# Kernel tuning notes

Hardware: AMD Instinct MI355X
Metric: run time of the kernel (lower is better)

Reference implementation:

```python
import jax, jax.numpy as jnp
import numpy as np

ASSIGN_RATIO = 0.1  # hard-coded inside coarsen_graph in the original
EPS_CUT = 1e-7
EPS_NORM = 1e-12  # torch F.normalize eps


def _normalize_batch_adj(adj):
    # adj: [B, N, N]
    n = adj.shape[1]
    A = adj + jnp.eye(n, dtype=adj.dtype)
    deg_inv_sqrt = jnp.clip(A.sum(-1), 1.0, None) ** -0.5  # [B, N]
    newA = deg_inv_sqrt[..., :, None] * A * deg_inv_sqrt[..., None, :]
    row_mask = (adj.sum(-1) > 0).astype(adj.dtype)  # [B, N]
    return row_mask[..., :, None] * newA


def setup_inputs():
    key = jax.random.key(0)
    k0, k1, k2, k3, k4 = jax.random.split(key, 5)
    B, N, D, T = 512, 128, 256, 512
    concept_hidden = jax.random.normal(k0, (B, N, D), jnp.float32)
    adj = jax.random.uniform(k1, (B, N, N), jnp.float32)
    head = jax.random.randint(k2, (B, T), 0, N)
    lin_w = jax.random.normal(k3, (1, D), jnp.float32) / np.sqrt(D).astype(np.float32)
    bias = jax.random.normal(k4, (1,), jnp.float32)
    return {"concept_hidden": concept_hidden, "adj": adj, "head": head,
            "lin_w": lin_w, "bias": bias}


def reference(concept_hidden, adj, head, lin_w, bias):
    # concept_hidden: [B, N, D], adj: [B, N, N], head: [B, T] node indices
    x = concept_hidden
    B, N, D = x.shape

    out = x @ lin_w.T                      # [B, N, 1]  self.lin(x)
    norm_adj = _normalize_batch_adj(adj)   # [B, N, N]
    out = norm_adj @ out + bias            # [B, N, 1]
    alpha = jax.nn.sigmoid(out ** 2)[..., 0]  # [B, N]

    # batch_num_nodes[i] = len(set(head[i]))  -> count unique via sort
    hs = jnp.sort(head, axis=-1)
    n_uniq = 1 + (hs[:, 1:] != hs[:, :-1]).sum(-1)  # [B]

    # per-sample k = ceil(n * 0.1) + 1 (only when n > 1); cut = k-th largest alpha
    k = jnp.ceil(n_uniq.astype(jnp.float32) * ASSIGN_RATIO).astype(jnp.int32) + 1
    a_desc = jnp.sort(alpha, axis=-1)[:, ::-1]       # descending
    idx = jnp.clip(k - 1, 0, N - 1)
    cut = jnp.take_along_axis(a_desc, idx[:, None], axis=-1)[:, 0]
    cut = jnp.where(n_uniq > 1, cut, jnp.zeros_like(cut))  # [B]

    cut_alpha = jax.nn.relu(alpha + EPS_CUT - cut[:, None])  # [B, N]

    # S = norm_adj * cut_alpha broadcast over rows, then L1-normalize rows
    S = norm_adj * cut_alpha[:, None, :]
    S = S / jnp.clip(jnp.abs(S).sum(-1, keepdims=True), EPS_NORM, None)

    St = jnp.swapaxes(S, 1, 2)             # [B, N, N]
    embedding_tensor = St @ x              # S^T x   [B, N, D]
    new_adj = (St @ adj) @ S               # S^T A S [B, N, N]
    return embedding_tensor, new_adj
```

## Files before the change

### kernel.cpp

```cpp
#include <hip/hip_runtime.h>

#define Bsz 512
#define Nn  128
#define Dd  256
#define Tt  512

typedef __attribute__((ext_vector_type(8))) short short8;
typedef __attribute__((ext_vector_type(4))) float f32x4;

__device__ __forceinline__ ushort f2bf(float f) {
    union { float f; unsigned u; } v; v.f = f;
    unsigned r = v.u + 0x7fffu + ((v.u >> 16) & 1u);
    return (ushort)(r >> 16);
}
__device__ __forceinline__ unsigned pk2(float a, float b) {
    return (unsigned)f2bf(a) | ((unsigned)f2bf(b) << 16);
}

__global__ __launch_bounds__(256) void xprep(
    const float* __restrict__ x, const float* __restrict__ lin_w,
    float* __restrict__ dotv2, ushort* __restrict__ xT)
{
    const int h = blockIdx.x, b = blockIdx.y;
    __shared__ float xbufT[32][130];
    __shared__ float pdot[128][8];
    __shared__ float wS[128];
    const int t = threadIdx.x;
    if (t < 128) wS[t] = lin_w[h * 128 + t];
    const int c4 = t & 7;
    const int kb = t >> 3;
    const int kc = t & 15, dsub = t >> 4;
    float p[4] = {0.f, 0.f, 0.f, 0.f};
    __syncthreads();

    for (int c = 0; c < 4; ++c) {
        const int dl = 4 * c4;
        float4 v[4];
#pragma unroll
        for (int i = 0; i < 4; ++i)
            v[i] = *(const float4*)&x[((size_t)b * Nn + (kb + 32 * i)) * Dd
                                      + h * 128 + c * 32 + dl];
        const float w0 = wS[c*32+dl],   w1 = wS[c*32+dl+1];
        const float w2 = wS[c*32+dl+2], w3 = wS[c*32+dl+3];
#pragma unroll
        for (int i = 0; i < 4; ++i) {
            p[i] += v[i].x*w0 + v[i].y*w1 + v[i].z*w2 + v[i].w*w3;
            xbufT[dl    ][kb + 32*i] = v[i].x;
            xbufT[dl + 1][kb + 32*i] = v[i].y;
            xbufT[dl + 2][kb + 32*i] = v[i].z;
            xbufT[dl + 3][kb + 32*i] = v[i].w;
        }
        __syncthreads();
#pragma unroll
        for (int pp = 0; pp < 2; ++pp) {
            int d = dsub + 16 * pp;
            float2 q0 = *(float2*)&xbufT[d][kc*8 + 0];
            float2 q1 = *(float2*)&xbufT[d][kc*8 + 2];
            float2 q2 = *(float2*)&xbufT[d][kc*8 + 4];
            float2 q3 = *(float2*)&xbufT[d][kc*8 + 6];
            uint4 pkv;
            pkv.x = pk2(q0.x, q0.y);
            pkv.y = pk2(q1.x, q1.y);
            pkv.z = pk2(q2.x, q2.y);
            pkv.w = pk2(q3.x, q3.y);
            *(uint4*)&xT[((size_t)b * Dd + h * 128 + c * 32 + d) * Nn + kc * 8] = pkv;
        }
        __syncthreads();
    }
#pragma unroll
    for (int i = 0; i < 4; ++i) pdot[kb + 32*i][c4] = p[i];
    __syncthreads();
    if (t < 128) {
        float s = 0.f;
#pragma unroll
        for (int j = 0; j < 8; ++j) s += pdot[t][j];
        dotv2[((size_t)b * Nn + t) * 2 + h] = s;
    }
}

__global__ __launch_bounds__(256) void sprep(
    const float* __restrict__ adj, const int* __restrict__ head,
    const float* __restrict__ dotv2, const float* __restrict__ bias,
    ushort* __restrict__ STbf)
{
    const int b = blockIdx.x;
    __shared__ __align__(16) float adjS[Nn][132];
    __shared__ __align__(16) float ttS[Nn], disS[Nn], maskS[Nn],
                                   alphaS[Nn], uS[Nn], rowcS[Nn];
    __shared__ float partS[Nn][2];
    __shared__ int   flags[Nn];
    __shared__ int   nuniq_s;
    __shared__ float cut_s;

    const int t = threadIdx.x;
    const float bias0 = bias[0];
    if (t < Nn) flags[t] = 0;
    if (t == 0) { nuniq_s = 0; cut_s = 0.f; }

    const float* adjb = adj + (size_t)b * (Nn * Nn);
#pragma unroll
    for (int i = 0; i < 16; ++i) {
        int f = t + 256 * i;
        int rr = f >> 5, c = (f & 31) * 4;
        *(float4*)&adjS[rr][c] = *(const float4*)&adjb[rr * Nn + c];
    }
    __syncthreads();

    {
        int h0 = head[(size_t)b * Tt + t];
        int h1 = head[(size_t)b * Tt + 256 + t];
        flags[h0] = 1; flags[h1] = 1;
    }

    const int r = t >> 1, hh = t & 1, base = hh * 64;
    {
        float4 s4 = {0.f, 0.f, 0.f, 0.f};
#pragma unroll
        for (int j = 0; j < 16; ++j) {
            float4 v = *(float4*)&adjS[r][base + 4*j];
            s4.x += v.x; s4.y += v.y; s4.z += v.z; s4.w += v.w;
        }
        partS[r][hh] = (s4.x + s4.y) + (s4.z + s4.w);
    }
    __syncthreads();
    if (t < Nn) {
        float rs  = partS[t][0] + partS[t][1];
        float m   = (rs > 0.f) ? 1.f : 0.f;
        float dis = 1.f / sqrtf(fmaxf(rs + 1.f, 1.f));
        maskS[t] = m; disS[t] = dis;
        float lin = dotv2[((size_t)b * Nn + t) * 2]
                  + dotv2[((size_t)b * Nn + t) * 2 + 1];
        ttS[t] = dis * lin;
        atomicAdd(&nuniq_s, flags[t]);
    }
    __syncthreads();
    {
        float4 a = {0.f, 0.f, 0.f, 0.f};
#pragma unroll
        for (int j = 0; j < 16; ++j) {
            float4 v = *(float4*)&adjS[r][base + 4*j];
            float4 w = *(float4*)&ttS[base + 4*j];
            a.x += v.x*w.x; a.y += v.y*w.y; a.z += v.z*w.z; a.w += v.w*w.w;
        }
        partS[r][hh] = (a.x + a.y) + (a.z + a.w);
    }
    __syncthreads();
    if (t < Nn) {
        float mv = partS[t][0] + partS[t][1];
        float o  = maskS[t] * disS[t] * (mv + ttS[t]) + bias0;
        alphaS[t] = 1.f / (1.f + expf(-o * o));
    }
    __syncthreads();
    if (t < Nn) {
        int nu = nuniq_s;
        if (nu > 1) {
            int idx = (int)ceilf((float)nu * 0.1f);
            if (idx > Nn - 1) idx = Nn - 1;
            float an = alphaS[t];
            int cg = 0, ce = 0;
            for (int j = 0; j < Nn; ++j) {
                float aj = alphaS[j];
                cg += (aj > an); ce += (aj == an);
            }
            if (cg <= idx && idx < cg + ce) cut_s = an;
        }
    }
    __syncthreads();
    if (t < Nn) uS[t] = fmaxf(alphaS[t] + 1e-7f - cut_s, 0.f) * disS[t];
    __syncthreads();
    {
        float4 a = {0.f, 0.f, 0.f, 0.f};
#pragma unroll
        for (int j = 0; j < 16; ++j) {
            float4 v = *(float4*)&adjS[r][base + 4*j];
            float4 w = *(float4*)&uS[base + 4*j];
            a.x += v.x*w.x; a.y += v.y*w.y; a.z += v.z*w.z; a.w += v.w*w.w;
        }
        partS[r][hh] = (a.x + a.y) + (a.z + a.w);
    }
    __syncthreads();
    if (t < Nn) {
        float tot  = partS[t][0] + partS[t][1] + uS[t];
        float rsum = maskS[t] * disS[t] * tot;
        rowcS[t] = maskS[t] * disS[t] / fmaxf(rsum, 1e-12f);
    }
    __syncthreads();
    {
        const float um = uS[r];
        ushort* outp = STbf + ((size_t)b * Nn + r) * Nn + base;
#pragma unroll
        for (int kcc = 0; kcc < 8; ++kcc) {
            int k0 = base + kcc * 8;
            float vv[8];
#pragma unroll
            for (int j = 0; j < 8; ++j) {
                int k = k0 + j;
                vv[j] = rowcS[k] * (adjS[k][r] + ((k == r) ? 1.f : 0.f)) * um;
            }
            uint4 pkv;
            pkv.x = pk2(vv[0], vv[1]); pkv.y = pk2(vv[2], vv[3]);
            pkv.z = pk2(vv[4], vv[5]); pkv.w = pk2(vv[6], vv[7]);
            *(uint4*)(outp + kcc * 8) = pkv;
        }
    }
}

__global__ __launch_bounds__(256, 2) void emb_gemm(
    const ushort* __restrict__ STbf, const ushort* __restrict__ xT,
    float* __restrict__ emb)
{
    const int d0 = blockIdx.x * 128;
    const int b  = blockIdx.y;
    __shared__ ushort STl[128][136];
    __shared__ ushort xTl[128][136];
    const int t = threadIdx.x;
    const uint4* sg = (const uint4*)(STbf + (size_t)b * Nn * Nn);
    const uint4* xg = (const uint4*)(xT + ((size_t)b * Dd + d0) * Nn);
#pragma unroll
    for (int i = 0; i < 8; ++i) {
        int f = t + 256 * i;
        int row = f >> 4, c8 = f & 15;
        *(uint4*)&STl[row][c8 * 8] = sg[f];
        *(uint4*)&xTl[row][c8 * 8] = xg[f];
    }
    __syncthreads();

    const int lane = t & 63, wv = t >> 6;
    const int l15 = lane & 15, quad = lane >> 4;
    const int m0 = wv * 32;
    f32x4 acc[2][8];
#pragma unroll
    for (int mt = 0; mt < 2; ++mt)
#pragma unroll
        for (int nt = 0; nt < 8; ++nt) acc[mt][nt] = (f32x4){0.f, 0.f, 0.f, 0.f};

#pragma unroll
    for (int k0 = 0; k0 < 128; k0 += 32) {
        short8 a0 = *(const short8*)&STl[m0 + l15][k0 + quad * 8];
        short8 a1 = *(const short8*)&STl[m0 + 16 + l15][k0 + quad * 8];
        short8 bf[8];
#pragma unroll
        for (int nt = 0; nt < 8; ++nt)
            bf[nt] = *(const short8*)&xTl[nt * 16 + l15][k0 + quad * 8];
#pragma unroll
        for (int nt = 0; nt < 8; ++nt) {
            acc[0][nt] = __builtin_amdgcn_mfma_f32_16x16x32_bf16(a0, bf[nt], acc[0][nt], 0, 0, 0);
            acc[1][nt] = __builtin_amdgcn_mfma_f32_16x16x32_bf16(a1, bf[nt], acc[1][nt], 0, 0, 0);
        }
    }
#pragma unroll
    for (int mt = 0; mt < 2; ++mt)
#pragma unroll
        for (int nt = 0; nt < 8; ++nt)
#pragma unroll
            for (int rr = 0; rr < 4; ++rr) {
                int row = m0 + mt * 16 + quad * 4 + rr;
                int col = d0 + nt * 16 + l15;
                emb[((size_t)b * Nn + row) * Dd + col] = acc[mt][nt][rr];
            }
}

__global__ __launch_bounds__(256, 2) void padj_gemm(
    const float* __restrict__ adj, const ushort* __restrict__ STbf,
    float* __restrict__ nadj)
{
    const int b = blockIdx.x;
    __shared__ ushort bufA[128][136];
    __shared__ ushort STl[128][136];
    const int t = threadIdx.x;

    const float* adjb = adj + (size_t)b * Nn * Nn;
#pragma unroll
    for (int i = 0; i < 16; ++i) {
        int f = t + 256 * i;
        int rr = f >> 5, c4 = f & 31;
        float4 v = *(const float4*)&adjb[rr * Nn + c4 * 4];
        uint2 w; w.x = pk2(v.x, v.y); w.y = pk2(v.z, v.w);
        *(uint2*)&bufA[rr][c4 * 4] = w;
    }
    const uint4* sg = (const uint4*)(STbf + (size_t)b * Nn * Nn);
#pragma unroll
    for (int i = 0; i < 8; ++i) {
        int f = t + 256 * i;
        *(uint4*)&STl[f >> 4][(f & 15) * 8] = sg[f];
    }
    __syncthreads();

    const int lane = t & 63, wv = t >> 6;
    const int l15 = lane & 15, quad = lane >> 4;
    const int m0 = wv * 32;
    f32x4 acc[2][8];
#pragma unroll
    for (int mt = 0; mt < 2; ++mt)
#pragma unroll
        for (int nt = 0; nt < 8; ++nt) acc[mt][nt] = (f32x4){0.f, 0.f, 0.f, 0.f};

#pragma unroll
    for (int k0 = 0; k0 < 128; k0 += 32) {
        short8 a0 = *(const short8*)&bufA[m0 + l15][k0 + quad * 8];
        short8 a1 = *(const short8*)&bufA[m0 + 16 + l15][k0 + quad * 8];
        short8 bf[8];
#pragma unroll
        for (int nt = 0; nt < 8; ++nt)
            bf[nt] = *(const short8*)&STl[nt * 16 + l15][k0 + quad * 8];
#pragma unroll
        for (int nt = 0; nt < 8; ++nt) {
            acc[0][nt] = __builtin_amdgcn_mfma_f32_16x16x32_bf16(a0, bf[nt], acc[0][nt], 0, 0, 0);
            acc[1][nt] = __builtin_amdgcn_mfma_f32_16x16x32_bf16(a1, bf[nt], acc[1][nt], 0, 0, 0);
        }
    }
    __syncthreads();
#pragma unroll
    for (int mt = 0; mt < 2; ++mt)
#pragma unroll
        for (int nt = 0; nt < 8; ++nt) {
            int j    = nt * 16 + l15;
            int mcol = m0 + mt * 16 + quad * 4;
            uint2 w;
            w.x = pk2(acc[mt][nt][0], acc[mt][nt][1]);
            w.y = pk2(acc[mt][nt][2], acc[mt][nt][3]);
            *(uint2*)&bufA[j][mcol] = w;
        }
    __syncthreads();

#pragma unroll
    for (int mt = 0; mt < 2; ++mt)
#pragma unroll
        for (int nt = 0; nt < 8; ++nt) acc[mt][nt] = (f32x4){0.f, 0.f, 0.f, 0.f};

#pragma unroll
    for (int k0 = 0; k0 < 128; k0 += 32) {
        short8 a0 = *(const short8*)&STl[m0 + l15][k0 + quad * 8];
        short8 a1 = *(const short8*)&STl[m0 + 16 + l15][k0 + quad * 8];
        short8 bf[8];
#pragma unroll
        for (int nt = 0; nt < 8; ++nt)
            bf[nt] = *(const short8*)&bufA[nt * 16 + l15][k0 + quad * 8];
#pragma unroll
        for (int nt = 0; nt < 8; ++nt) {
            acc[0][nt] = __builtin_amdgcn_mfma_f32_16x16x32_bf16(a0, bf[nt], acc[0][nt], 0, 0, 0);
            acc[1][nt] = __builtin_amdgcn_mfma_f32_16x16x32_bf16(a1, bf[nt], acc[1][nt], 0, 0, 0);
        }
    }
#pragma unroll
    for (int mt = 0; mt < 2; ++mt)
#pragma unroll
        for (int nt = 0; nt < 8; ++nt)
#pragma unroll
            for (int rr = 0; rr < 4; ++rr) {
                int row = m0 + mt * 16 + quad * 4 + rr;
                int col = nt * 16 + l15;
                nadj[((size_t)b * Nn + row) * Nn + col] = acc[mt][nt][rr];
            }
}

extern "C" void kernel_launch(void* const* d_in, const int* in_sizes, int n_in,
                              void* d_out, int out_size, void* d_ws, size_t ws_size,
                              hipStream_t stream)
{
    const float* x     = (const float*)d_in[0];
    const float* adj   = (const float*)d_in[1];
    const int*   head  = (const int*)d_in[2];
    const float* lin_w = (const float*)d_in[3];
    const float* bias  = (const float*)d_in[4];

    float* emb  = (float*)d_out;
    float* nadj = emb + (size_t)Bsz * Nn * Dd;

    ushort* STbf = (ushort*)d_ws;
    ushort* xT   = STbf + (size_t)Bsz * Nn * Nn;
    float*  dotv2 = (float*)(xT + (size_t)Bsz * Dd * Nn);

    xprep<<<dim3(2, Bsz), 256, 0, stream>>>(x, lin_w, dotv2, xT);
    sprep<<<Bsz, 256, 0, stream>>>(adj, head, dotv2, bias, STbf);
    emb_gemm<<<dim3(2, Bsz), 256, 0, stream>>>(STbf, xT, emb);
    padj_gemm<<<Bsz, 256, 0, stream>>>(adj, STbf, nadj);
}
```

Baseline: 230.6 us.

## Fuse four per-batch kernels into one mega kernel keeping S and adj in LDS

Merges xprep, sprep, emb_gemm and padj_gemm into a single kernel with one block per batch. The fp32 adjacency stays in shared memory and S^T goes straight to LDS as bf16, so the global workspace round-trips for STbf, xT and dotv2 and three extra launches disappear. x is read twice (once for the lin dot, once transposed through LDS for the embedding GEMM). This brings less parallelism (512 blocks instead of 1024 for the emb GEMM), larger LDS use per block and a longer serial chain of stages inside each block.

```diff
diff --git a/kernel.cpp b/kernel.cpp
--- a/kernel.cpp
+++ b/kernel.cpp
@@ -16,131 +16,90 @@
 __device__ __forceinline__ unsigned pk2(float a, float b) {
     return (unsigned)f2bf(a) | ((unsigned)f2bf(b) << 16);
 }
-
-__global__ __launch_bounds__(256) void xprep(
-    const float* __restrict__ x, const float* __restrict__ lin_w,
-    float* __restrict__ dotv2, ushort* __restrict__ xT)
+__device__ __forceinline__ short8 pk8(const float* v) {
+    union { uint4 u; short8 s; } c;
+    c.u.x = pk2(v[0], v[1]); c.u.y = pk2(v[2], v[3]);
+    c.u.z = pk2(v[4], v[5]); c.u.w = pk2(v[6], v[7]);
+    return c.s;
+}
+
+__global__ __launch_bounds__(256) void mega(
+    const float* __restrict__ x, const float* __restrict__ adj,
+    const int* __restrict__ head, const float* __restrict__ lin_w,
+    const float* __restrict__ bias,
+    float* __restrict__ emb, float* __restrict__ nadj)
 {
-    const int h = blockIdx.x, b = blockIdx.y;
-    __shared__ float xbufT[32][130];
-    __shared__ float pdot[128][8];
-    __shared__ float wS[128];
-    const int t = threadIdx.x;
-    if (t < 128) wS[t] = lin_w[h * 128 + t];
-    const int c4 = t & 7;
-    const int kb = t >> 3;
-    const int kc = t & 15, dsub = t >> 4;
-    float p[4] = {0.f, 0.f, 0.f, 0.f};
-    __syncthreads();
-
-    for (int c = 0; c < 4; ++c) {
-        const int dl = 4 * c4;
-        float4 v[4];
-#pragma unroll
-        for (int i = 0; i < 4; ++i)
-            v[i] = *(const float4*)&x[((size_t)b * Nn + (kb + 32 * i)) * Dd
-                                      + h * 128 + c * 32 + dl];
-        const float w0 = wS[c*32+dl],   w1 = wS[c*32+dl+1];
-        const float w2 = wS[c*32+dl+2], w3 = wS[c*32+dl+3];
-#pragma unroll
-        for (int i = 0; i < 4; ++i) {
-            p[i] += v[i].x*w0 + v[i].y*w1 + v[i].z*w2 + v[i].w*w3;
-            xbufT[dl    ][kb + 32*i] = v[i].x;
-            xbufT[dl + 1][kb + 32*i] = v[i].y;
-            xbufT[dl + 2][kb + 32*i] = v[i].z;
-            xbufT[dl + 3][kb + 32*i] = v[i].w;
-        }
-        __syncthreads();
-#pragma unroll
-        for (int pp = 0; pp < 2; ++pp) {
-            int d = dsub + 16 * pp;
-            float2 q0 = *(float2*)&xbufT[d][kc*8 + 0];
-            float2 q1 = *(float2*)&xbufT[d][kc*8 + 2];
-            float2 q2 = *(float2*)&xbufT[d][kc*8 + 4];
-            float2 q3 = *(float2*)&xbufT[d][kc*8 + 6];
-            uint4 pkv;
-            pkv.x = pk2(q0.x, q0.y);
-            pkv.y = pk2(q1.x, q1.y);
-            pkv.z = pk2(q2.x, q2.y);
-            pkv.w = pk2(q3.x, q3.y);
-            *(uint4*)&xT[((size_t)b * Dd + h * 128 + c * 32 + d) * Nn + kc * 8] = pkv;
-        }
-        __syncthreads();
-    }
-#pragma unroll
-    for (int i = 0; i < 4; ++i) pdot[kb + 32*i][c4] = p[i];
-    __syncthreads();
-    if (t < 128) {
-        float s = 0.f;
-#pragma unroll
-        for (int j = 0; j < 8; ++j) s += pdot[t][j];
-        dotv2[((size_t)b * Nn + t) * 2 + h] = s;
-    }
-}
-
-__global__ __launch_bounds__(256) void sprep(
-    const float* __restrict__ adj, const int* __restrict__ head,
-    const float* __restrict__ dotv2, const float* __restrict__ bias,
-    ushort* __restrict__ STbf)
-{
-    const int b = blockIdx.x;
-    __shared__ __align__(16) float adjS[Nn][132];
-    __shared__ __align__(16) float ttS[Nn], disS[Nn], maskS[Nn],
-                                   alphaS[Nn], uS[Nn], rowcS[Nn];
+    const int b = blockIdx.x, t = threadIdx.x;
+    __shared__ __align__(16) float bufA[Nn][132];
+    __shared__ __align__(16) ushort STl[Nn][136];
+    __shared__ float wS[Dd];
+    __shared__ float ttS[Nn], disS[Nn], maskS[Nn], alphaS[Nn], uS[Nn], rowcS[Nn];
     __shared__ float partS[Nn][2];
+    __shared__ float dotP[Nn][2];
     __shared__ int   flags[Nn];
-    __shared__ int   nuniq_s;
-    __shared__ float cut_s;
-
-    const int t = threadIdx.x;
+    __shared__ int   nuniq;
+    __shared__ float cutS;
+
     const float bias0 = bias[0];
+    wS[t] = lin_w[t];
     if (t < Nn) flags[t] = 0;
-    if (t == 0) { nuniq_s = 0; cut_s = 0.f; }
-
-    const float* adjb = adj + (size_t)b * (Nn * Nn);
+    if (t == 0) { nuniq = 0; cutS = 0.f; }
+
+    const float* adjb = adj + (size_t)b * Nn * Nn;
 #pragma unroll
     for (int i = 0; i < 16; ++i) {
         int f = t + 256 * i;
         int rr = f >> 5, c = (f & 31) * 4;
-        *(float4*)&adjS[rr][c] = *(const float4*)&adjb[rr * Nn + c];
-    }
-    __syncthreads();
-
-    {
-        int h0 = head[(size_t)b * Tt + t];
-        int h1 = head[(size_t)b * Tt + 256 + t];
-        flags[h0] = 1; flags[h1] = 1;
-    }
-
-    const int r = t >> 1, hh = t & 1, base = hh * 64;
+        *(float4*)&bufA[rr][c] = *(const float4*)&adjb[(size_t)rr * Nn + c];
+    }
+    __syncthreads();
+
+    { int h0 = head[(size_t)b * Tt + t];
+      int h1 = head[(size_t)b * Tt + 256 + t];
+      flags[h0] = 1; flags[h1] = 1; }
+
+    {
+        const int dr = t >> 1, dh = t & 1;
+        const float4* xr = (const float4*)(x + ((size_t)b * Nn + dr) * Dd + dh * 128);
+        float p = 0.f;
+#pragma unroll 8
+        for (int i = 0; i < 32; ++i) {
+            float4 v = xr[i];
+            const float* w = &wS[dh * 128 + 4 * i];
+            p += v.x * w[0] + v.y * w[1] + v.z * w[2] + v.w * w[3];
+        }
+        dotP[dr][dh] = p;
+    }
+
+    const int r = t >> 1, hh = t & 1, cb = hh * 64;
     {
         float4 s4 = {0.f, 0.f, 0.f, 0.f};
 #pragma unroll
         for (int j = 0; j < 16; ++j) {
-            float4 v = *(float4*)&adjS[r][base + 4*j];
+            float4 v = *(float4*)&bufA[r][cb + 4 * j];
             s4.x += v.x; s4.y += v.y; s4.z += v.z; s4.w += v.w;
         }
         partS[r][hh] = (s4.x + s4.y) + (s4.z + s4.w);
     }
     __syncthreads();
+
     if (t < Nn) {
         float rs  = partS[t][0] + partS[t][1];
-        float m   = (rs > 0.f) ? 1.f : 0.f;
+        maskS[t]  = (rs > 0.f) ? 1.f : 0.f;
         float dis = 1.f / sqrtf(fmaxf(rs + 1.f, 1.f));
-        maskS[t] = m; disS[t] = dis;
-        float lin = dotv2[((size_t)b * Nn + t) * 2]
-                  + dotv2[((size_t)b * Nn + t) * 2 + 1];
-        ttS[t] = dis * lin;
-        atomicAdd(&nuniq_s, flags[t]);
-    }
-    __syncthreads();
+        disS[t]   = dis;
+        ttS[t]    = dis * (dotP[t][0] + dotP[t][1]);
+        atomicAdd(&nuniq, flags[t]);
+    }
+    __syncthreads();
+
     {
         float4 a = {0.f, 0.f, 0.f, 0.f};
 #pragma unroll
         for (int j = 0; j < 16; ++j) {
-            float4 v = *(float4*)&adjS[r][base + 4*j];
-            float4 w = *(float4*)&ttS[base + 4*j];
-            a.x += v.x*w.x; a.y += v.y*w.y; a.z += v.z*w.z; a.w += v.w*w.w;
+            float4 v = *(float4*)&bufA[r][cb + 4 * j];
+            float4 w = *(float4*)&ttS[cb + 4 * j];
+            a.x += v.x * w.x; a.y += v.y * w.y; a.z += v.z * w.z; a.w += v.w * w.w;
         }
         partS[r][hh] = (a.x + a.y) + (a.z + a.w);
     }
@@ -152,7 +111,7 @@
     }
     __syncthreads();
     if (t < Nn) {
-        int nu = nuniq_s;
+        int nu = nuniq;
         if (nu > 1) {
             int idx = (int)ceilf((float)nu * 0.1f);
             if (idx > Nn - 1) idx = Nn - 1;
@@ -162,19 +121,19 @@
                 float aj = alphaS[j];
                 cg += (aj > an); ce += (aj == an);
             }
-            if (cg <= idx && idx < cg + ce) cut_s = an;
-        }
-    }
-    __syncthreads();
-    if (t < Nn) uS[t] = fmaxf(alphaS[t] + 1e-7f - cut_s, 0.f) * disS[t];
+            if (cg <= idx && idx < cg + ce) cutS = an;
+        }
+    }
+    __syncthreads();
+    if (t < Nn) uS[t] = fmaxf(alphaS[t] + 1e-7f - cutS, 0.f) * disS[t];
     __syncthreads();
     {
         float4 a = {0.f, 0.f, 0.f, 0.f};
 #pragma unroll
         for (int j = 0; j < 16; ++j) {
-            float4 v = *(float4*)&adjS[r][base + 4*j];
-            float4 w = *(float4*)&uS[base + 4*j];
-            a.x += v.x*w.x; a.y += v.y*w.y; a.z += v.z*w.z; a.w += v.w*w.w;
+            float4 v = *(float4*)&bufA[r][cb + 4 * j];
+            float4 w = *(float4*)&uS[cb + 4 * j];
+            a.x += v.x * w.x; a.y += v.y * w.y; a.z += v.z * w.z; a.w += v.w * w.w;
         }
         partS[r][hh] = (a.x + a.y) + (a.z + a.w);
     }
@@ -182,46 +141,27 @@
     if (t < Nn) {
         float tot  = partS[t][0] + partS[t][1] + uS[t];
         float rsum = maskS[t] * disS[t] * tot;
-        rowcS[t] = maskS[t] * disS[t] / fmaxf(rsum, 1e-12f);
-    }
-    __syncthreads();
-    {
-        const float um = uS[r];
-        ushort* outp = STbf + ((size_t)b * Nn + r) * Nn + base;
-#pragma unroll
-        for (int kcc = 0; kcc < 8; ++kcc) {
-            int k0 = base + kcc * 8;
+        rowcS[t]   = maskS[t] * disS[t] / fmaxf(rsum, 1e-12f);
+    }
+    __syncthreads();
+
+    {
+        const int m = r;
+        const float um = uS[m];
+#pragma unroll
+        for (int kc = 0; kc < 8; ++kc) {
+            int k0 = cb + kc * 8;
             float vv[8];
 #pragma unroll
             for (int j = 0; j < 8; ++j) {
                 int k = k0 + j;
-                vv[j] = rowcS[k] * (adjS[k][r] + ((k == r) ? 1.f : 0.f)) * um;
+                vv[j] = rowcS[k] * (bufA[k][m] + ((k == m) ? 1.f : 0.f)) * um;
             }
             uint4 pkv;
             pkv.x = pk2(vv[0], vv[1]); pkv.y = pk2(vv[2], vv[3]);
             pkv.z = pk2(vv[4], vv[5]); pkv.w = pk2(vv[6], vv[7]);
-            *(uint4*)(outp + kcc * 8) = pkv;
-        }
-    }
-}
-
-__global__ __launch_bounds__(256, 2) void emb_gemm(
-    const ushort* __restrict__ STbf, const ushort* __restrict__ xT,
-    float* __restrict__ emb)
-{
-    const int d0 = blockIdx.x * 128;
-    const int b  = blockIdx.y;
-    __shared__ ushort STl[128][136];
-    __shared__ ushort xTl[128][136];
-    const int t = threadIdx.x;
-    const uint4* sg = (const uint4*)(STbf + (size_t)b * Nn * Nn);
-    const uint4* xg = (const uint4*)(xT + ((size_t)b * Dd + d0) * Nn);
-#pragma unroll
-    for (int i = 0; i < 8; ++i) {
-        int f = t + 256 * i;
-        int row = f >> 4, c8 = f & 15;
-        *(uint4*)&STl[row][c8 * 8] = sg[f];
-        *(uint4*)&xTl[row][c8 * 8] = xg[f];
+            *(uint4*)&STl[m][k0] = pkv;
+        }
     }
     __syncthreads();
 
@@ -236,80 +176,26 @@
 
 #pragma unroll
     for (int k0 = 0; k0 < 128; k0 += 32) {
-        short8 a0 = *(const short8*)&STl[m0 + l15][k0 + quad * 8];
-        short8 a1 = *(const short8*)&STl[m0 + 16 + l15][k0 + quad * 8];
+        float av[8];
+        *(float4*)&av[0] = *(float4*)&bufA[m0 + l15][k0 + quad * 8];
+        *(float4*)&av[4] = *(float4*)&bufA[m0 + l15][k0 + quad * 8 + 4];
+        short8 a0 = pk8(av);
+        *(float4*)&av[0] = *(float4*)&bufA[m0 + 16 + l15][k0 + quad * 8];
+        *(float4*)&av[4] = *(float4*)&bufA[m0 + 16 + l15][k0 + quad * 8 + 4];
+        short8 a1 = pk8(av);
         short8 bf[8];
 #pragma unroll
         for (int nt = 0; nt < 8; ++nt)
-            bf[nt] = *(const short8*)&xTl[nt * 16 + l15][k0 + quad * 8];
+            bf[nt] = *(const short8*)&STl[nt * 16 + l15][k0 + quad * 8];
 #pragma unroll
         for (int nt = 0; nt < 8; ++nt) {
             acc[0][nt] = __builtin_amdgcn_mfma_f32_16x16x32_bf16(a0, bf[nt], acc[0][nt], 0, 0, 0);
             acc[1][nt] = __builtin_amdgcn_mfma_f32_16x16x32_bf16(a1, bf[nt], acc[1][nt], 0, 0, 0);
         }
     }
-#pragma unroll
-    for (int mt = 0; mt < 2; ++mt)
-#pragma unroll
-        for (int nt = 0; nt < 8; ++nt)
-#pragma unroll
-            for (int rr = 0; rr < 4; ++rr) {
-                int row = m0 + mt * 16 + quad * 4 + rr;
-                int col = d0 + nt * 16 + l15;
-                emb[((size_t)b * Nn + row) * Dd + col] = acc[mt][nt][rr];
-            }
-}
-
-__global__ __launch_bounds__(256, 2) void padj_gemm(
-    const float* __restrict__ adj, const ushort* __restrict__ STbf,
-    float* __restrict__ nadj)
-{
-    const int b = blockIdx.x;
-    __shared__ ushort bufA[128][136];
-    __shared__ ushort STl[128][136];
-    const int t = threadIdx.x;
-
-    const float* adjb = adj + (size_t)b * Nn * Nn;
-#pragma unroll
-    for (int i = 0; i < 16; ++i) {
-        int f = t + 256 * i;
-        int rr = f >> 5, c4 = f & 31;
-        float4 v = *(const float4*)&adjb[rr * Nn + c4 * 4];
-        uint2 w; w.x = pk2(v.x, v.y); w.y = pk2(v.z, v.w);
-        *(uint2*)&bufA[rr][c4 * 4] = w;
-    }
-    const uint4* sg = (const uint4*)(STbf + (size_t)b * Nn * Nn);
-#pragma unroll
-    for (int i = 0; i < 8; ++i) {
-        int f = t + 256 * i;
-        *(uint4*)&STl[f >> 4][(f & 15) * 8] = sg[f];
-    }
-    __syncthreads();
-
-    const int lane = t & 63, wv = t >> 6;
-    const int l15 = lane & 15, quad = lane >> 4;
-    const int m0 = wv * 32;
-    f32x4 acc[2][8];
-#pragma unroll
-    for (int mt = 0; mt < 2; ++mt)
-#pragma unroll
-        for (int nt = 0; nt < 8; ++nt) acc[mt][nt] = (f32x4){0.f, 0.f, 0.f, 0.f};
-
-#pragma unroll
-    for (int k0 = 0; k0 < 128; k0 += 32) {
-        short8 a0 = *(const short8*)&bufA[m0 + l15][k0 + quad * 8];
-        short8 a1 = *(const short8*)&bufA[m0 + 16 + l15][k0 + quad * 8];
-        short8 bf[8];
-#pragma unroll
-        for (int nt = 0; nt < 8; ++nt)
-            bf[nt] = *(const short8*)&STl[nt * 16 + l15][k0 + quad * 8];
-#pragma unroll
-        for (int nt = 0; nt < 8; ++nt) {
-            acc[0][nt] = __builtin_amdgcn_mfma_f32_16x16x32_bf16(a0, bf[nt], acc[0][nt], 0, 0, 0);
-            acc[1][nt] = __builtin_amdgcn_mfma_f32_16x16x32_bf16(a1, bf[nt], acc[1][nt], 0, 0, 0);
-        }
-    }
-    __syncthreads();
+    __syncthreads();
+
+    ushort (*PT)[136] = (ushort(*)[136])&bufA[0][0];
 #pragma unroll
     for (int mt = 0; mt < 2; ++mt)
 #pragma unroll
@@ -319,7 +205,7 @@
             uint2 w;
             w.x = pk2(acc[mt][nt][0], acc[mt][nt][1]);
             w.y = pk2(acc[mt][nt][2], acc[mt][nt][3]);
-            *(uint2*)&bufA[j][mcol] = w;
+            *(uint2*)&PT[j][mcol] = w;
         }
     __syncthreads();
 
@@ -335,7 +221,7 @@
         short8 bf[8];
 #pragma unroll
         for (int nt = 0; nt < 8; ++nt)
-            bf[nt] = *(const short8*)&bufA[nt * 16 + l15][k0 + quad * 8];
+            bf[nt] = *(const short8*)&PT[nt * 16 + l15][k0 + quad * 8];
 #pragma unroll
         for (int nt = 0; nt < 8; ++nt) {
             acc[0][nt] = __builtin_amdgcn_mfma_f32_16x16x32_bf16(a0, bf[nt], acc[0][nt], 0, 0, 0);
@@ -352,6 +238,59 @@
                 int col = nt * 16 + l15;
                 nadj[((size_t)b * Nn + row) * Nn + col] = acc[mt][nt][rr];
             }
+    __syncthreads();
+
+    float (*xbufF)[132] = (float(*)[132])&bufA[0][0];
+    short8 aE[2][4];
+#pragma unroll
+    for (int ks = 0; ks < 4; ++ks) {
+        aE[0][ks] = *(const short8*)&STl[m0 + l15][ks * 32 + quad * 8];
+        aE[1][ks] = *(const short8*)&STl[m0 + 16 + l15][ks * 32 + quad * 8];
+    }
+    for (int qd = 0; qd < 4; ++qd) {
+        const int d0 = qd * 64;
+#pragma unroll
+        for (int i = 0; i < 8; ++i) {
+            int f = t + 256 * i;
+            int k = f >> 4, c4 = (f & 15) * 4;
+            float4 v = *(const float4*)&x[((size_t)b * Nn + k) * Dd + d0 + c4];
+            xbufF[c4    ][k] = v.x; xbufF[c4 + 1][k] = v.y;
+            xbufF[c4 + 2][k] = v.z; xbufF[c4 + 3][k] = v.w;
+        }
+        __syncthreads();
+        f32x4 accE[2][4];
+#pragma unroll
+        for (int mt = 0; mt < 2; ++mt)
+#pragma unroll
+            for (int nt = 0; nt < 4; ++nt) accE[mt][nt] = (f32x4){0.f, 0.f, 0.f, 0.f};
+#pragma unroll
+        for (int ks = 0; ks < 4; ++ks) {
+            short8 bf[4];
+#pragma unroll
+            for (int nt = 0; nt < 4; ++nt) {
+                float bv[8];
+                *(float4*)&bv[0] = *(float4*)&xbufF[nt * 16 + l15][ks * 32 + quad * 8];
+                *(float4*)&bv[4] = *(float4*)&xbufF[nt * 16 + l15][ks * 32 + quad * 8 + 4];
+                bf[nt] = pk8(bv);
+            }
+#pragma unroll
+            for (int nt = 0; nt < 4; ++nt) {
+                accE[0][nt] = __builtin_amdgcn_mfma_f32_16x16x32_bf16(aE[0][ks], bf[nt], accE[0][nt], 0, 0, 0);
+                accE[1][nt] = __builtin_amdgcn_mfma_f32_16x16x32_bf16(aE[1][ks], bf[nt], accE[1][nt], 0, 0, 0);
+            }
+        }
+#pragma unroll
+        for (int mt = 0; mt < 2; ++mt)
+#pragma unroll
+            for (int nt = 0; nt < 4; ++nt)
+#pragma unroll
+                for (int rr = 0; rr < 4; ++rr) {
+                    int row = m0 + mt * 16 + quad * 4 + rr;
+                    int col = d0 + nt * 16 + l15;
+                    emb[((size_t)b * Nn + row) * Dd + col] = accE[mt][nt][rr];
+                }
+        __syncthreads();
+    }
 }
 
 extern "C" void kernel_launch(void* const* d_in, const int* in_sizes, int n_in,
@@ -367,12 +306,5 @@
     float* emb  = (float*)d_out;
     float* nadj = emb + (size_t)Bsz * Nn * Dd;
 
-    ushort* STbf = (ushort*)d_ws;
-    ushort* xT   = STbf + (size_t)Bsz * Nn * Nn;
-    float*  dotv2 = (float*)(xT + (size_t)Bsz * Dd * Nn);
-
-    xprep<<<dim3(2, Bsz), 256, 0, stream>>>(x, lin_w, dotv2, xT);
-    sprep<<<Bsz, 256, 0, stream>>>(adj, head, dotv2, bias, STbf);
-    emb_gemm<<<dim3(2, Bsz), 256, 0, stream>>>(STbf, xT, emb);
-    padj_gemm<<<Bsz, 256, 0, stream>>>(adj, STbf, nadj);
-}
+    mega<<<Bsz, 256, 0, stream>>>(x, adj, head, lin_w, bias, emb, nadj);
+}
```

Result: faster. 217.4 us (-5.7%).
